# Kernel tuning notes

Hardware: AMD Instinct MI355X
Metric: run time of the kernel (lower is better)

## Reference

```python
import jax, jax.numpy as jnp
import numpy as np

NUM_GROUPS = 16
GN_EPS = 1e-5
POOL = 4
CLAMP_MIN, CLAMP_MAX = 0.0, 1.0


def setup_inputs() -> dict:
    key = jax.random.key(0)
    k = jax.random.split(key, 4)
    x = jax.random.normal(k[0], (128, 8, 128, 128), dtype=jnp.float32)
    conv_weight = jax.random.normal(k[1], (64, 8, 3, 3), dtype=jnp.float32) * 0.1
    conv_bias = jax.random.normal(k[2], (64,), dtype=jnp.float32) * 0.1
    gn_weight = jnp.ones((64,), dtype=jnp.float32)
    gn_bias = jnp.zeros((64,), dtype=jnp.float32)
    scale = jax.random.normal(k[3], (64, 1, 1), dtype=jnp.float32)
    return {"x": x, "conv_weight": conv_weight, "conv_bias": conv_bias,
            "gn_weight": gn_weight, "gn_bias": gn_bias, "scale": scale}


def reference(x, conv_weight, conv_bias, gn_weight, gn_bias, scale):
    # Conv2d 3x3, stride 1, padding 0 (torch defaults). NCHW / OIHW.
    y = jax.lax.conv_general_dilated(
        x, conv_weight, window_strides=(1, 1), padding='VALID',
        dimension_numbers=('NCHW', 'OIHW', 'NCHW'))
    y = y + conv_bias[None, :, None, None]  # [N, 64, 126, 126]

    # GroupNorm(16 groups over 64 channels): stats over (C//G, H, W) per group.
    N, C, H, W = y.shape
    g = y.reshape(N, NUM_GROUPS, C // NUM_GROUPS, H, W)
    mean = jnp.mean(g, axis=(2, 3, 4), keepdims=True)
    var = jnp.mean(jnp.square(g - mean), axis=(2, 3, 4), keepdims=True)
    g = (g - mean) * jax.lax.rsqrt(var + GN_EPS)
    y = g.reshape(N, C, H, W) * gn_weight[None, :, None, None] + gn_bias[None, :, None, None]

    # Per-channel scale (scale has shape [64, 1, 1], broadcasts over H, W).
    y = y * scale[None]

    # MaxPool2d(kernel=4, stride=4), floor mode -> 126 // 4 = 31.
    y = jax.lax.reduce_window(
        y, -jnp.inf, jax.lax.max,
        window_dimensions=(1, 1, POOL, POOL),
        window_strides=(1, 1, POOL, POOL), padding='VALID')

    # Clamp.
    return jnp.clip(y, CLAMP_MIN, CLAMP_MAX)
```

## Files before the change

### kernel.cpp

```cpp
#include <hip/hip_runtime.h>
#include <hip/hip_fp16.h>

namespace {
constexpr int ICH = 8, IH = 128, IW = 128;
constexpr int CPG = 4, PH = 31;
constexpr int ICS = 516;
constexpr float EPS = 1e-5f;
constexpr float MPX = 126.f * 126.f;
constexpr int TOTAL_OUT = 128 * 64 * PH * PH;
constexpr size_t WS_NEED = (size_t)128 * 16 * 8 * 2 * 4;

typedef _Float16 v8h __attribute__((ext_vector_type(8)));
typedef float v4f __attribute__((ext_vector_type(4)));
typedef unsigned short u16;
typedef unsigned int u32;

__device__ __forceinline__ void gll16(const void* g, void* l) {
  __builtin_amdgcn_global_load_lds((const __attribute__((address_space(1))) void*)g,
                                   (__attribute__((address_space(3))) void*)l, 16, 0, 0);
}

__device__ __forceinline__ u32 pkh(float a, float b) {
  unsigned short lo = __half_as_ushort(__float2half_rn(a));
  unsigned short hi = __half_as_ushort(__float2half_rn(b));
  return (u32)lo | ((u32)hi << 16);
}

__global__ __launch_bounds__(256, 2) void conv_mfma(
    const float* __restrict__ x, const float* __restrict__ cw,
    const float* __restrict__ cb, const float* __restrict__ gnw,
    const float* __restrict__ sc, float* __restrict__ out,
    float* __restrict__ wsp) {
  __shared__ __align__(16) u16 ring[12][1056];

  const int bid = blockIdx.x;
  const int n = bid >> 3, e = bid & 7;
  const int out_lo = e * 16;
  const int out_hi = (e == 7) ? 125 : out_lo + 15;
  const int NST = (e == 7) ? 4 : 5;
  const int t = threadIdx.x;
  const int w = t >> 6, l = t & 63;
  const int colB = l & 15, qt = l >> 4;

  for (int idx = t; idx < 12 * 32; idx += 256)
    ring[idx >> 5][1024 + (idx & 31)] = 0;

  const int ocA = 16 * w + colB;
  const float flipA = (gnw[ocA] * sc[ocA] >= 0.f) ? 1.f : -1.f;
  v8h af[3];
#pragma unroll
  for (int kc = 0; kc < 3; ++kc) {
    const int tap = kc * 4 + qt;
#pragma unroll
    for (int i = 0; i < 8; ++i)
      af[kc][i] = (tap < 9) ? (_Float16)(flipA * cw[ocA * 72 + i * 9 + tap])
                            : (_Float16)0.f;
  }
  int eofc[3], dhl[3];
#pragma unroll
  for (int kc = 0; kc < 3; ++kc) {
    int tap = kc * 4 + qt; tap = (tap > 8) ? 8 : tap;
    dhl[kc] = tap / 3;
    eofc[kc] = (colB + tap % 3) * 8;
  }
  float flip[4];
#pragma unroll
  for (int q = 0; q < 4; ++q) {
    int oc = 16 * w + qt * 4 + q;
    flip[q] = (gnw[oc] * sc[oc] >= 0.f) ? 1.f : -1.f;
  }
  const u16* rb = &ring[0][0];

  const int prg = t >> 7;
  const int px = t & 127;
  const float* xb = x + ((size_t)n * ICH) * (IH * IW) + px;
  float fs[16];
  auto load_regs = [&](int s) {
#pragma unroll
    for (int rr = 0; rr < 2; ++rr) {
      const int grow = out_lo + 4 * s + 2 * prg + rr;
      const float* gp = xb + (size_t)grow * IW;
#pragma unroll
      for (int ic = 0; ic < 8; ++ic)
        fs[rr * 8 + ic] = gp[(size_t)ic * (IH * IW)];
    }
  };
  auto write_lds = [&](int s) {
#pragma unroll
    for (int rr = 0; rr < 2; ++rr) {
      const int grow = out_lo + 4 * s + 2 * prg + rr;
      const int slot = grow % 12;
      uint4 v;
      v.x = pkh(fs[rr * 8 + 0], fs[rr * 8 + 1]);
      v.y = pkh(fs[rr * 8 + 2], fs[rr * 8 + 3]);
      v.z = pkh(fs[rr * 8 + 4], fs[rr * 8 + 5]);
      v.w = pkh(fs[rr * 8 + 6], fs[rr * 8 + 7]);
      *reinterpret_cast<uint4*>(&ring[slot][px * 8]) = v;
    }
  };

  load_regs(0);
  write_lds(0);

  float s1q[4] = {0.f, 0.f, 0.f, 0.f};
  float s2g = 0.f;
  float pacc[8][4];
#pragma unroll
  for (int ci = 0; ci < 8; ++ci)
#pragma unroll
    for (int q = 0; q < 4; ++q) pacc[ci][q] = -3.4e38f;

  for (int s = 0; s < NST; ++s) {
    __syncthreads();
    if (s + 1 < NST) load_regs(s + 1);
#pragma unroll
    for (int ri = 0; ri < 4; ++ri) {
      const int r = out_lo + 4 * s - 2 + ri;
      if (r < out_lo || r > out_hi) continue;
      const int rm = r % 12;
      int eoff[3];
#pragma unroll
      for (int kc = 0; kc < 3; ++kc) {
        int sl = rm + dhl[kc];
        if (sl >= 12) sl -= 12;
        eoff[kc] = sl * 1056 + eofc[kc];
      }
#pragma unroll
      for (int ci = 0; ci < 8; ++ci) {
        v4f acc = {0.f, 0.f, 0.f, 0.f};
#pragma unroll
        for (int kc = 0; kc < 3; ++kc) {
          v8h bf = *reinterpret_cast<const v8h*>(rb + eoff[kc] + ci * 128);
          acc = __builtin_amdgcn_mfma_f32_16x16x32_f16(af[kc], bf, acc, 0, 0, 0);
        }
        if (ci < 7) {
#pragma unroll
          for (int q = 0; q < 4; ++q) {
            s1q[q] += acc[q];
            s2g = fmaf(acc[q], acc[q], s2g);
            pacc[ci][q] = fmaxf(pacc[ci][q], acc[q]);
          }
        } else {
          const bool va = (colB < 14);
#pragma unroll
          for (int q = 0; q < 4; ++q) {
            float a = va ? acc[q] : 0.f;
            s1q[q] += a;
            s2g = fmaf(a, a, s2g);
            float fv = va ? acc[q] : -3.4e38f;
            pacc[7][q] = fmaxf(pacc[7][q], fv);
          }
        }
      }
      if ((r & 3) == 3) {
        const int pr = r >> 2;
        float* ob = out + (((size_t)n * 64 + 16 * w + qt * 4) * PH + pr) * PH;
#pragma unroll
        for (int ci = 0; ci < 8; ++ci) {
#pragma unroll
          for (int q = 0; q < 4; ++q) {
            float pm = pacc[ci][q];
            pm = fmaxf(pm, __shfl_xor(pm, 1, 64));
            pm = fmaxf(pm, __shfl_xor(pm, 2, 64));
            if ((l & 3) == 0 && (ci < 7 || colB < 12)) {
              int pc = ci * 4 + (colB >> 2);
              ob[(size_t)q * (PH * PH) + pc] = flip[q] * pm;
            }
            pacc[ci][q] = -3.4e38f;
          }
        }
      }
    }
    if (s + 1 < NST) write_lds(s + 1);
  }

#pragma unroll
  for (int off = 1; off <= 8; off <<= 1) {
#pragma unroll
    for (int q = 0; q < 4; ++q) s1q[q] += __shfl_xor(s1q[q], off, 64);
    s2g += __shfl_xor(s2g, off, 64);
  }
  if ((l & 15) == 0) {
    const float cnte = 126.f * (float)(out_hi - out_lo + 1);
    float S1 = 0.f, S2 = s2g;
#pragma unroll
    for (int q = 0; q < 4; ++q) {
      float s1t = flip[q] * s1q[q];
      float b = cb[16 * w + qt * 4 + q];
      S1 += s1t + cnte * b;
      S2 += 2.f * b * s1t + cnte * b * b;
    }
    int g = 4 * w + qt;
    float* wp = wsp + ((size_t)(n * 16 + g) * 8 + e) * 2;
    wp[0] = S1; wp[1] = S2;
  }
}

__global__ __launch_bounds__(256) void gn_affine_clamp(
    float* __restrict__ out, const float* __restrict__ wsp,
    const float* __restrict__ gnw, const float* __restrict__ gnb,
    const float* __restrict__ sc, const float* __restrict__ cb) {
  int i = blockIdx.x * 256 + threadIdx.x;
  const int stride = gridDim.x * 256;
  for (; i < TOTAL_OUT; i += stride) {
    int c = (i / 961) & 63;
    int n = i / 61504;
    const float* wp = wsp + ((size_t)(n * 16 + (c >> 2)) * 8) * 2;
    float S1 = 0.f, S2 = 0.f;
#pragma unroll
    for (int e = 0; e < 8; ++e) { S1 += wp[2 * e]; S2 += wp[2 * e + 1]; }
    constexpr float invN = 1.f / (4.f * MPX);
    float mean = S1 * invN;
    float var = S2 * invN - mean * mean;
    float inv = rsqrtf(var + EPS);
    float gw = gnw[c];
    float A = gw * inv * sc[c];
    float B = (gnb[c] - mean * inv * gw) * sc[c] + A * cb[c];
    float v = fmaf(A, out[i], B);
    out[i] = fminf(fmaxf(v, 0.f), 1.f);
  }
}

#define FIN(T, DOSTATS, RE)                                                    \
  {                                                                            \
    float f0 = T[0] + __shfl_xor(T[0], 32, 64);                                \
    float f1 = T[1] + __shfl_xor(T[1], 32, 64);                                \
    float f2 = T[2] + __shfl_xor(T[2], 32, 64);                                \
    float f3 = T[3] + __shfl_xor(T[3], 32, 64);                                \
    if (DOSTATS) {                                                             \
      s1 += f0 + f1 + m23 * (f2 + f3);                                         \
      float qa = fmaf(f0, f0, f1 * f1);                                        \
      float qb = fmaf(f2, f2, f3 * f3);                                        \
      s2 += qa + m23 * qb;                                                     \
    }                                                                          \
    RE = fmaxf(fmaxf(flip * f0, flip * f1), fmaxf(flip * f2, flip * f3));      \
  }
#define ZERO(T) { T[0] = 0.f; T[1] = 0.f; T[2] = 0.f; T[3] = 0.f; }
#define ROWF(RR, T2, T1, T0)                                                   \
  {                                                                            \
    _Pragma("unroll") for (int i4 = 0; i4 < 4; ++i4) {                         \
      const float* rp = bp + (4 * p + i4) * ICS + (RR) * IW + 4 * j;           \
      float4 v4 = *reinterpret_cast<const float4*>(rp);                        \
      float2 v2 = *reinterpret_cast<const float2*>(rp + 4);                    \
      float in[6] = {v4.x, v4.y, v4.z, v4.w, v2.x, v2.y};                      \
      _Pragma("unroll") for (int dw = 0; dw < 3; ++dw) {                       \
        const float w0 = wf[i4 * 9 + dw];                                      \
        const float w1 = wf[i4 * 9 + 3 + dw];                                  \
        const float w2 = wf[i4 * 9 + 6 + dw];                                  \
        _Pragma("unroll") for (int q = 0; q < 4; ++q) {                        \
          T2[q] = fmaf(in[q + dw], w2, T2[q]);                                 \
          T1[q] = fmaf(in[q + dw], w1, T1[q]);                                 \
          T0[q] = fmaf(in[q + dw], w0, T0[q]);                                 \
        }                                                                      \
      }                                                                        \
    }                                                                          \
  }
#define STAGEF(S, X, Y, Z, DOS01, DOWIN)                                       \
  {                                                                            \
    __syncthreads();                                                           \
    const int cur = (S) & 1;                                                   \
    if ((S) < 31) issue(4 * ((S) + 1), cur ^ 1);                               \
    const float* bp = &buf[cur][0][0];                                         \
    float re0, re1, re2, re3;                                                  \
    ROWF(0, X, Y, Z) FIN(X, DOS01, re0) ZERO(X)                                \
    ROWF(1, Y, Z, X) FIN(Y, DOS01, re1) ZERO(Y)                                \
    if (DOWIN) {                                                               \
      float wfin = fmaxf(wprev, fmaxf(re0, re1));                              \
      if (p == 0 && j < 31) mm[c][(S) - 1][j] = __float2half(flip * wfin);     \
    }                                                                          \
    ROWF(2, Z, X, Y) FIN(Z, true, re2) ZERO(Z)                                 \
    ROWF(3, X, Y, Z) FIN(X, true, re3) ZERO(X)                                 \
    wprev = fmaxf(re2, re3);                                                   \
  }

__global__ __launch_bounds__(256, 2) void fused_conv_gn_pool_f32(
    const float* __restrict__ x, const float* __restrict__ cw,
    const float* __restrict__ cb, const float* __restrict__ gnw,
    const float* __restrict__ gnb, const float* __restrict__ sc,
    float* __restrict__ out) {
  __shared__ float buf[2][ICH][ICS];
  __shared__ __half mm[CPG][PH][PH];
  __shared__ float red[8];
  __shared__ float stats[2];

  const int bid = blockIdx.x;
  const int xcd = bid & 7;
  const int kb = bid >> 3;
  const int n = xcd * 16 + (kb >> 4);
  const int g = kb & 15;
  const int t = threadIdx.x;
  const int c = t >> 6;
  const int u = t & 63;
  const int p = u >> 5;
  const int j = u & 31;
  const int gc = g * CPG + c;

  float wf[36];
  {
    const float4* wp = reinterpret_cast<const float4*>(cw + gc * 72 + p * 36);
#pragma unroll
    for (int q = 0; q < 9; ++q) {
      float4 v = wp[q];
      wf[4 * q + 0] = v.x; wf[4 * q + 1] = v.y;
      wf[4 * q + 2] = v.z; wf[4 * q + 3] = v.w;
    }
  }
  const float flip = ((gnw[gc] * sc[gc]) >= 0.f) ? 1.f : -1.f;
  const float m23 = (j < 31) ? 1.f : 0.f;

  const float* xn = x + (size_t)n * ICH * IH * IW;

  auto issue = [&](int br, int which) {
#pragma unroll
    for (int k = 0; k < 4; ++k) {
      const int m = c * 4 + k;
      const int ic = m >> 1;
      const int r2 = (m & 1) * 2;
      const float* gp = xn + (size_t)(ic * IH + br + r2) * IW + u * 4;
      gll16(gp, &buf[which][ic][r2 * IW]);
    }
  };

  issue(0, 0);

  float s1 = 0.f, s2 = 0.f, wprev = 0.f;
  float A0[4] = {0, 0, 0, 0}, A1[4] = {0, 0, 0, 0}, A2[4] = {0, 0, 0, 0};

  STAGEF(0, A0, A1, A2, false, false)
  for (int s = 1; s <= 28; s += 3) {
    STAGEF(s,     A1, A2, A0, true, true)
    STAGEF(s + 1, A2, A0, A1, true, true)
    STAGEF(s + 2, A0, A1, A2, true, true)
  }
  STAGEF(31, A1, A2, A0, true, true)

#pragma unroll
  for (int off = 32; off > 0; off >>= 1) {
    s1 += __shfl_down(s1, off, 64);
    s2 += __shfl_down(s2, off, 64);
  }
  const float bc = cb[gc];
  if (u == 0) {
    float t1 = 0.5f * s1, t2 = 0.5f * s2;
    red[c * 2] = t1 + MPX * bc;
    red[c * 2 + 1] = t2 + 2.f * bc * t1 + MPX * bc * bc;
  }
  __syncthreads();
  if (t == 0) {
    float S1 = red[0] + red[2] + red[4] + red[6];
    float S2 = red[1] + red[3] + red[5] + red[7];
    constexpr float invN = 1.f / (CPG * 126.f * 126.f);
    float mean = S1 * invN;
    float var = S2 * invN - mean * mean;
    stats[0] = mean;
    stats[1] = rsqrtf(var + EPS);
  }
  __syncthreads();
  const float mean = stats[0], inv = stats[1];

  float* outp = out + ((size_t)n * 64 + g * CPG) * (PH * PH);
  for (int kk = 0; kk < 16; ++kk) {
    int idx = t + kk * 256;
    if (idx < CPG * PH * PH) {
      int cc = idx / (PH * PH);
      int rem = idx - cc * (PH * PH);
      float e = __half2float(mm[cc][rem / PH][rem % PH]);
      int gcc = g * CPG + cc;
      float gw = gnw[gcc];
      float A = gw * inv * sc[gcc];
      float B = (gnb[gcc] - mean * inv * gw) * sc[gcc] + A * cb[gcc];
      float v = fmaf(A, e, B);
      v = fminf(fmaxf(v, 0.f), 1.f);
      outp[cc * (PH * PH) + rem] = v;
    }
  }
}
}

extern "C" void kernel_launch(void* const* d_in, const int* in_sizes, int n_in,
                              void* d_out, int out_size, void* d_ws, size_t ws_size,
                              hipStream_t stream) {
  const float* x   = (const float*)d_in[0];
  const float* cw  = (const float*)d_in[1];
  const float* cb  = (const float*)d_in[2];
  const float* gnw = (const float*)d_in[3];
  const float* gnb = (const float*)d_in[4];
  const float* sc  = (const float*)d_in[5];
  float* out = (float*)d_out;

  if (ws_size >= WS_NEED) {
    float* wsp = (float*)d_ws;
    hipLaunchKernelGGL(conv_mfma, dim3(1024), dim3(256), 0, stream,
                       x, cw, cb, gnw, sc, out, wsp);
    hipLaunchKernelGGL(gn_affine_clamp, dim3(2048), dim3(256), 0, stream,
                       out, wsp, gnw, gnb, sc, cb);
  } else {
    hipLaunchKernelGGL(fused_conv_gn_pool_f32, dim3(2048), dim3(256), 0, stream,
                       x, cw, cb, gnw, gnb, sc, out);
  }
}
```

Baseline: 91.63 us.

## Switch conv to 32x32x16 MFMA with 512-thread blocks and LDS stat reduction

Replaces the 16x16x32 f16 MFMA conv tiling with 32x32x16 MFMAs. Each wave now covers 32 output channels by 32 pixels using 5 K-chunks that pair two taps each, and the block grows to 512 threads so eight waves split channels and pixel tiles. Global loads per thread are halved, sign flips become a bitmask, and the GroupNorm partial sums are combined across waves through shared memory before being written out. The aim is fewer MFMA issues and higher per-instruction throughput. In exchange, one of the ten tap slots is wasted as zero padding, the last pixel tile is partly masked, and the 4-blocks-per-CU launch bound may raise register pressure.

After: 165.6 us. +80.7%, slower.

```diff
diff --git a/kernel.cpp b/kernel.cpp
--- a/kernel.cpp
+++ b/kernel.cpp
@@ -12,6 +12,7 @@
 
 typedef _Float16 v8h __attribute__((ext_vector_type(8)));
 typedef float v4f __attribute__((ext_vector_type(4)));
+typedef float v16f __attribute__((ext_vector_type(16)));
 typedef unsigned short u16;
 typedef unsigned int u32;
 
@@ -26,12 +27,13 @@
   return (u32)lo | ((u32)hi << 16);
 }
 
-__global__ __launch_bounds__(256, 2) void conv_mfma(
+__global__ __launch_bounds__(512, 4) void conv_mfma(
     const float* __restrict__ x, const float* __restrict__ cw,
     const float* __restrict__ cb, const float* __restrict__ gnw,
     const float* __restrict__ sc, float* __restrict__ out,
     float* __restrict__ wsp) {
   __shared__ __align__(16) u16 ring[12][1056];
+  __shared__ float red[16][4][2];
 
   const int bid = blockIdx.x;
   const int n = bid >> 3, e = bid & 7;
@@ -40,75 +42,70 @@
   const int NST = (e == 7) ? 4 : 5;
   const int t = threadIdx.x;
   const int w = t >> 6, l = t & 63;
-  const int colB = l & 15, qt = l >> 4;
-
-  for (int idx = t; idx < 12 * 32; idx += 256)
+  const int ptile = w & 3, h = w >> 2;
+  const int hi5 = l >> 5;
+  const int pxl = 32 * ptile + (l & 31);
+
+  for (int idx = t; idx < 12 * 32; idx += 512)
     ring[idx >> 5][1024 + (idx & 31)] = 0;
 
-  const int ocA = 16 * w + colB;
+  const int ocA = 32 * h + (l & 31);
   const float flipA = (gnw[ocA] * sc[ocA] >= 0.f) ? 1.f : -1.f;
-  v8h af[3];
-#pragma unroll
-  for (int kc = 0; kc < 3; ++kc) {
-    const int tap = kc * 4 + qt;
+  v8h af[5];
+#pragma unroll
+  for (int kc = 0; kc < 5; ++kc) {
+    const int tap = 2 * kc + hi5;
 #pragma unroll
     for (int i = 0; i < 8; ++i)
       af[kc][i] = (tap < 9) ? (_Float16)(flipA * cw[ocA * 72 + i * 9 + tap])
                             : (_Float16)0.f;
   }
-  int eofc[3], dhl[3];
-#pragma unroll
-  for (int kc = 0; kc < 3; ++kc) {
-    int tap = kc * 4 + qt; tap = (tap > 8) ? 8 : tap;
-    dhl[kc] = tap / 3;
-    eofc[kc] = (colB + tap % 3) * 8;
-  }
-  float flip[4];
-#pragma unroll
-  for (int q = 0; q < 4; ++q) {
-    int oc = 16 * w + qt * 4 + q;
-    flip[q] = (gnw[oc] * sc[oc] >= 0.f) ? 1.f : -1.f;
-  }
+  int eofc[5], dhl[5];
+#pragma unroll
+  for (int kc = 0; kc < 5; ++kc) {
+    const int tap = 2 * kc + hi5;
+    if (tap <= 8) {
+      dhl[kc] = tap / 3;
+      eofc[kc] = (pxl + tap % 3) * 8;
+    } else {
+      dhl[kc] = 0;
+      eofc[kc] = 0;
+    }
+  }
+  u32 fb = 0;
+#pragma unroll
+  for (int reg = 0; reg < 16; ++reg) {
+    const int oc = 32 * h + (reg & 3) + 8 * (reg >> 2) + 4 * hi5;
+    if (gnw[oc] * sc[oc] < 0.f) fb |= (1u << reg);
+  }
+  const float mv = (pxl < 126) ? 1.f : 0.f;
   const u16* rb = &ring[0][0];
 
-  const int prg = t >> 7;
-  const int px = t & 127;
-  const float* xb = x + ((size_t)n * ICH) * (IH * IW) + px;
-  float fs[16];
+  const int srow = t >> 7;
+  const int spx = t & 127;
+  const float* xb = x + (size_t)n * ICH * IH * IW + spx;
+  float fs[8];
   auto load_regs = [&](int s) {
-#pragma unroll
-    for (int rr = 0; rr < 2; ++rr) {
-      const int grow = out_lo + 4 * s + 2 * prg + rr;
-      const float* gp = xb + (size_t)grow * IW;
-#pragma unroll
-      for (int ic = 0; ic < 8; ++ic)
-        fs[rr * 8 + ic] = gp[(size_t)ic * (IH * IW)];
-    }
+    const int grow = out_lo + 4 * s + srow;
+    const float* gp = xb + (size_t)grow * IW;
+#pragma unroll
+    for (int ic = 0; ic < 8; ++ic) fs[ic] = gp[(size_t)ic * (IH * IW)];
   };
   auto write_lds = [&](int s) {
-#pragma unroll
-    for (int rr = 0; rr < 2; ++rr) {
-      const int grow = out_lo + 4 * s + 2 * prg + rr;
-      const int slot = grow % 12;
-      uint4 v;
-      v.x = pkh(fs[rr * 8 + 0], fs[rr * 8 + 1]);
-      v.y = pkh(fs[rr * 8 + 2], fs[rr * 8 + 3]);
-      v.z = pkh(fs[rr * 8 + 4], fs[rr * 8 + 5]);
-      v.w = pkh(fs[rr * 8 + 6], fs[rr * 8 + 7]);
-      *reinterpret_cast<uint4*>(&ring[slot][px * 8]) = v;
-    }
+    const int grow = out_lo + 4 * s + srow;
+    const int slot = grow % 12;
+    uint4 v;
+    v.x = pkh(fs[0], fs[1]); v.y = pkh(fs[2], fs[3]);
+    v.z = pkh(fs[4], fs[5]); v.w = pkh(fs[6], fs[7]);
+    *reinterpret_cast<uint4*>(&ring[slot][spx * 8]) = v;
   };
 
   load_regs(0);
   write_lds(0);
 
-  float s1q[4] = {0.f, 0.f, 0.f, 0.f};
-  float s2g = 0.f;
-  float pacc[8][4];
-#pragma unroll
-  for (int ci = 0; ci < 8; ++ci)
-#pragma unroll
-    for (int q = 0; q < 4; ++q) pacc[ci][q] = -3.4e38f;
+  float s1[16], pacc[16], s2[4] = {0.f, 0.f, 0.f, 0.f};
+#pragma unroll
+  for (int reg = 0; reg < 16; ++reg) { s1[reg] = 0.f; pacc[reg] = -3.4e38f; }
 
   for (int s = 0; s < NST; ++s) {
     __syncthreads();
@@ -118,56 +115,44 @@
       const int r = out_lo + 4 * s - 2 + ri;
       if (r < out_lo || r > out_hi) continue;
       const int rm = r % 12;
-      int eoff[3];
-#pragma unroll
-      for (int kc = 0; kc < 3; ++kc) {
+      int eoff[5];
+#pragma unroll
+      for (int kc = 0; kc < 5; ++kc) {
         int sl = rm + dhl[kc];
         if (sl >= 12) sl -= 12;
         eoff[kc] = sl * 1056 + eofc[kc];
       }
-#pragma unroll
-      for (int ci = 0; ci < 8; ++ci) {
-        v4f acc = {0.f, 0.f, 0.f, 0.f};
-#pragma unroll
-        for (int kc = 0; kc < 3; ++kc) {
-          v8h bf = *reinterpret_cast<const v8h*>(rb + eoff[kc] + ci * 128);
-          acc = __builtin_amdgcn_mfma_f32_16x16x32_f16(af[kc], bf, acc, 0, 0, 0);
-        }
-        if (ci < 7) {
-#pragma unroll
-          for (int q = 0; q < 4; ++q) {
-            s1q[q] += acc[q];
-            s2g = fmaf(acc[q], acc[q], s2g);
-            pacc[ci][q] = fmaxf(pacc[ci][q], acc[q]);
-          }
-        } else {
-          const bool va = (colB < 14);
-#pragma unroll
-          for (int q = 0; q < 4; ++q) {
-            float a = va ? acc[q] : 0.f;
-            s1q[q] += a;
-            s2g = fmaf(a, a, s2g);
-            float fv = va ? acc[q] : -3.4e38f;
-            pacc[7][q] = fmaxf(pacc[7][q], fv);
-          }
-        }
+      v16f acc = {0.f, 0.f, 0.f, 0.f, 0.f, 0.f, 0.f, 0.f,
+                  0.f, 0.f, 0.f, 0.f, 0.f, 0.f, 0.f, 0.f};
+#pragma unroll
+      for (int kc = 0; kc < 5; ++kc) {
+        v8h bf = *reinterpret_cast<const v8h*>(rb + eoff[kc]);
+        acc = __builtin_amdgcn_mfma_f32_32x32x16_f16(af[kc], bf, acc, 0, 0, 0);
+      }
+#pragma unroll
+      for (int reg = 0; reg < 16; ++reg) {
+        const float v = acc[reg];
+        const float am = mv * v;
+        s1[reg] += am;
+        s2[reg >> 2] = fmaf(am, am, s2[reg >> 2]);
+        pacc[reg] = fmaxf(pacc[reg], v);
       }
       if ((r & 3) == 3) {
         const int pr = r >> 2;
-        float* ob = out + (((size_t)n * 64 + 16 * w + qt * 4) * PH + pr) * PH;
-#pragma unroll
-        for (int ci = 0; ci < 8; ++ci) {
-#pragma unroll
-          for (int q = 0; q < 4; ++q) {
-            float pm = pacc[ci][q];
-            pm = fmaxf(pm, __shfl_xor(pm, 1, 64));
-            pm = fmaxf(pm, __shfl_xor(pm, 2, 64));
-            if ((l & 3) == 0 && (ci < 7 || colB < 12)) {
-              int pc = ci * 4 + (colB >> 2);
-              ob[(size_t)q * (PH * PH) + pc] = flip[q] * pm;
-            }
-            pacc[ci][q] = -3.4e38f;
+        const int pc = 8 * ptile + ((l & 31) >> 2);
+        const bool writer = ((l & 3) == 0) && (pc < 31);
+#pragma unroll
+        for (int reg = 0; reg < 16; ++reg) {
+          float pm = pacc[reg];
+          pm = fmaxf(pm, __shfl_xor(pm, 1, 64));
+          pm = fmaxf(pm, __shfl_xor(pm, 2, 64));
+          if (writer) {
+            const int oc = 32 * h + (reg & 3) + 8 * (reg >> 2) + 4 * hi5;
+            const u32 sm = (fb << (31 - reg)) & 0x80000000u;
+            out[(((size_t)n * 64 + oc) * PH + pr) * PH + pc] =
+                __uint_as_float(__float_as_uint(pm) ^ sm);
           }
+          pacc[reg] = -3.4e38f;
         }
       }
     }
@@ -175,23 +160,37 @@
   }
 
 #pragma unroll
-  for (int off = 1; off <= 8; off <<= 1) {
-#pragma unroll
-    for (int q = 0; q < 4; ++q) s1q[q] += __shfl_xor(s1q[q], off, 64);
-    s2g += __shfl_xor(s2g, off, 64);
-  }
-  if ((l & 15) == 0) {
-    const float cnte = 126.f * (float)(out_hi - out_lo + 1);
-    float S1 = 0.f, S2 = s2g;
-#pragma unroll
-    for (int q = 0; q < 4; ++q) {
-      float s1t = flip[q] * s1q[q];
-      float b = cb[16 * w + qt * 4 + q];
-      S1 += s1t + cnte * b;
-      S2 += 2.f * b * s1t + cnte * b * b;
-    }
-    int g = 4 * w + qt;
-    float* wp = wsp + ((size_t)(n * 16 + g) * 8 + e) * 2;
+  for (int off = 1; off <= 16; off <<= 1) {
+#pragma unroll
+    for (int reg = 0; reg < 16; ++reg) s1[reg] += __shfl_xor(s1[reg], off, 64);
+#pragma unroll
+    for (int j = 0; j < 4; ++j) s2[j] += __shfl_xor(s2[j], off, 64);
+  }
+  if ((l & 31) == 0) {
+    const float rows_e = (float)(out_hi - out_lo + 1);
+    const float cnt_w = (ptile == 3 ? 30.f : 32.f) * rows_e;
+#pragma unroll
+    for (int j = 0; j < 4; ++j) {
+      float S1 = 0.f, S2 = s2[j];
+#pragma unroll
+      for (int q = 0; q < 4; ++q) {
+        const int reg = 4 * j + q;
+        const int oc = 32 * h + q + 8 * j + 4 * hi5;
+        const float su = (fb & (1u << reg)) ? -s1[reg] : s1[reg];
+        const float b = cb[oc];
+        S1 += su + cnt_w * b;
+        S2 += 2.f * b * su + cnt_w * b * b;
+      }
+      const int g = 8 * h + 2 * j + hi5;
+      red[g][ptile][0] = S1;
+      red[g][ptile][1] = S2;
+    }
+  }
+  __syncthreads();
+  if (t < 16) {
+    const float S1 = red[t][0][0] + red[t][1][0] + red[t][2][0] + red[t][3][0];
+    const float S2 = red[t][0][1] + red[t][1][1] + red[t][2][1] + red[t][3][1];
+    float* wp = wsp + ((size_t)(n * 16 + t) * 8 + e) * 2;
     wp[0] = S1; wp[1] = S2;
   }
 }
@@ -390,7 +389,7 @@
 
   if (ws_size >= WS_NEED) {
     float* wsp = (float*)d_ws;
-    hipLaunchKernelGGL(conv_mfma, dim3(1024), dim3(256), 0, stream,
+    hipLaunchKernelGGL(conv_mfma, dim3(1024), dim3(512), 0, stream,
                        x, cw, cb, gnw, sc, out, wsp);
     hipLaunchKernelGGL(gn_affine_clamp, dim3(2048), dim3(256), 0, stream,
                        out, wsp, gnw, gnb, sc, cb);
```
